# Performance work log

Hardware: AMD Instinct MI355X
Metric: run time of the kernel (lower is better)

## Reference

```python
import jax, jax.numpy as jnp
import numpy as np

N = 100000
F_IN = 128
HID = 128
NCLS = 40
NEG_SLOPE = 0.2
BN_EPS = 1e-5


def setup_inputs() -> dict:
    key = jax.random.key(0)
    ks = jax.random.split(key, 16)
    x = jax.random.normal(ks[0], (N, F_IN), dtype=jnp.float32)
    # self-loop-free random edges: dst = (src + 1 + r) % N
    E = 1600000
    src = jax.random.randint(ks[1], (E,), 0, N)
    off = jax.random.randint(ks[2], (E,), 1, N)
    dst = (src + off) % N
    edge_index = jnp.stack([src, dst]).astype(jnp.int64)

    def glorot(k, shape):
        fan = shape[0] + shape[-1]
        s = jnp.sqrt(6.0 / fan)
        return jax.random.uniform(k, shape, jnp.float32, -s, s)

    params = {
        'W1': glorot(ks[3], (F_IN, HID)),
        'as1': glorot(ks[4], (HID,)), 'ad1': glorot(ks[5], (HID,)),
        'b1': jnp.zeros((HID,), jnp.float32),
        'g1': jnp.ones((HID,), jnp.float32), 'beta1': jnp.zeros((HID,), jnp.float32),
        'W2': glorot(ks[6], (HID, HID)),
        'as2': glorot(ks[7], (HID,)), 'ad2': glorot(ks[8], (HID,)),
        'b2': jnp.zeros((HID,), jnp.float32),
        'g2': jnp.ones((HID,), jnp.float32), 'beta2': jnp.zeros((HID,), jnp.float32),
        'Wc': glorot(ks[9], (HID, NCLS)),
        'bc': jnp.zeros((NCLS,), jnp.float32),
    }
    return {'x': x, 'edge_index': edge_index, **params}


def _gat_conv(h_in, src, dst, W, a_src, a_dst, bias):
    # heads=1, concat=False -> single head, mean over heads is identity
    h = h_in @ W                               # [N, C]
    alpha_s = h @ a_src                        # [N]
    alpha_d = h @ a_dst                        # [N]
    alpha = alpha_s[src] + alpha_d[dst]        # [E] edge score
    alpha = jax.nn.leaky_relu(alpha, NEG_SLOPE)
    # segment softmax over destination node neighborhoods
    m = jax.ops.segment_max(alpha, dst, num_segments=N)
    e = jnp.exp(alpha - m[dst])
    s = jax.ops.segment_sum(e, dst, num_segments=N)
    alpha = e / s[dst]
    msg = h[src] * alpha[:, None]              # [E, C]
    out = jax.ops.segment_sum(msg, dst, num_segments=N)
    return out + bias


def _batchnorm(x, gamma, beta):
    mu = jnp.mean(x, axis=0)
    var = jnp.mean(jnp.square(x - mu), axis=0)  # biased, as torch BN training
    return (x - mu) * jax.lax.rsqrt(var + BN_EPS) * gamma + beta


def reference(x, edge_index, W1, as1, ad1, b1, g1, beta1,
              W2, as2, ad2, b2, g2, beta2, Wc, bc):
    src, dst = edge_index[0], edge_index[1]
    # add self loops (input edges are guaranteed self-loop-free)
    loop = jnp.arange(N, dtype=src.dtype)
    src = jnp.concatenate([src, loop])
    dst = jnp.concatenate([dst, loop])

    h = _gat_conv(x, src, dst, W1, as1, ad1, b1)
    h = jax.nn.relu(_batchnorm(h, g1, beta1))
    h = _gat_conv(h, src, dst, W2, as2, ad2, b2)
    h = jax.nn.relu(_batchnorm(h, g2, beta2))
    return h @ Wc + bc
```

## Files before the change

### kernel.cpp

```cpp
#include <hip/hip_runtime.h>
#include <hip/hip_fp16.h>
#include <math.h>


#define CDIM 128
#define NCLS_ 40
#define NEG_SLOPE_ 0.2f
#define BN_EPS_ 1e-5f
#define BRNG 256
#define BCAP 6144
#define EPB 16

using short8  = __attribute__((ext_vector_type(8))) short;
using short4v = __attribute__((ext_vector_type(4))) short;
using f32x4   = __attribute__((ext_vector_type(4))) float;

static __device__ __forceinline__ float lrelu(float a) {
    return a > 0.f ? a : NEG_SLOPE_ * a;
}
static __device__ __forceinline__ short f2bf(float f) {
    unsigned u = __float_as_uint(f);
    u += 0x7fffu + ((u >> 16) & 1u);
    return (short)(u >> 16);
}
static __device__ __forceinline__ float bf_lo(unsigned u) { return __uint_as_float(u << 16); }
static __device__ __forceinline__ float bf_hi(unsigned u) { return __uint_as_float(u & 0xffff0000u); }
static __device__ __forceinline__ __half2 u2h2(unsigned u) { return __builtin_bit_cast(__half2, u); }
static __device__ __forceinline__ unsigned h22u(__half2 h) { return __builtin_bit_cast(unsigned, h); }

__global__ void k_setup(int* bcur, float* bnsum, int NB, int n, int E, int* offs,
                        const float* __restrict__ W1, const float* __restrict__ W2,
                        const float* __restrict__ Wc,
                        short* __restrict__ Wt1, short* __restrict__ Wt2,
                        short* __restrict__ Wtc) {
    int i = blockIdx.x * blockDim.x + threadIdx.x;
    if (i < NB) bcur[i] = 0;
    if (i < 512) bnsum[i] = 0.f;
    if (i == 0) offs[n] = E + n;
    if (i < 128 * 128) {
        int k = i >> 7, nn = i & 127;
        Wt1[nn * 128 + k] = f2bf(W1[i]);
        Wt2[nn * 128 + k] = f2bf(W2[i]);
    }
    if (i < 48 * 128) {
        int nn = i >> 7, k = i & 127;
        Wtc[i] = (nn < NCLS_) ? f2bf(Wc[k * NCLS_ + nn]) : (short)0;
    }
}

__global__ __launch_bounds__(256) void k_binA(
    const int* __restrict__ src, const int* __restrict__ dst, int E,
    int* __restrict__ bcur, uint2* __restrict__ bucket, int NB)
{
    __shared__ int hist[400];
    __shared__ int base[400];
    int t = threadIdx.x;
    long e0 = (long)blockIdx.x * (256 * EPB) + t;

    for (int i = t; i < NB; i += 256) hist[i] = 0;
    __syncthreads();

    int sv[EPB], dv[EPB];
    #pragma unroll
    for (int i = 0; i < EPB; i++) {
        long e = e0 + (long)i * 256;
        if (e < E) {
            sv[i] = src[e]; dv[i] = dst[e];
            atomicAdd(&hist[dv[i] >> 8], 1);
        } else dv[i] = -1;
    }
    __syncthreads();

    for (int i = t; i < NB; i += 256) {
        int h = hist[i];
        base[i] = (h > 0) ? atomicAdd(&bcur[i], h) : 0;
    }
    __syncthreads();
    for (int i = t; i < NB; i += 256) hist[i] = 0;
    __syncthreads();

    #pragma unroll
    for (int i = 0; i < EPB; i++) {
        if (dv[i] >= 0) {
            int b = dv[i] >> 8;
            int pos = base[b] + atomicAdd(&hist[b], 1);
            if (pos < BCAP)
                bucket[(size_t)b * BCAP + pos] =
                    make_uint2((unsigned)sv[i], (unsigned)dv[i]);
        }
    }
}

__global__ __launch_bounds__(256) void k_fillB(
    const uint2* __restrict__ bucket, const int* __restrict__ bcur,
    int n, int NB, int* __restrict__ offs, int* __restrict__ csr)
{
    __shared__ int hist[256];
    __shared__ int scanb[256];
    __shared__ int cur[256];
    __shared__ int buf[BCAP + BRNG];
    int b = blockIdx.x, t = threadIdx.x;
    int node0 = b << 8;
    int nodesIn = min(BRNG, n - node0);
    int cnt = min(bcur[b], BCAP);
    const uint2* mybkt = bucket + (size_t)b * BCAP;

    int part = 0;
    for (int j = t; j < b; j += 256) part += min(bcur[j], BCAP);
    scanb[t] = part; __syncthreads();
    for (int s2 = 128; s2 > 0; s2 >>= 1) {
        if (t < s2) scanb[t] += scanb[t + s2];
        __syncthreads();
    }
    int base = scanb[0] + node0;
    __syncthreads();

    hist[t] = 0; __syncthreads();
    for (int e2 = t; e2 < cnt; e2 += 256)
        atomicAdd(&hist[mybkt[e2].y & 255], 1);
    __syncthreads();

    int v = hist[t] + ((t < nodesIn) ? 1 : 0);
    scanb[t] = v; __syncthreads();
    for (int d = 1; d < 256; d <<= 1) {
        int x2 = (t >= d) ? scanb[t - d] : 0;
        __syncthreads();
        scanb[t] += x2;
        __syncthreads();
    }
    int lo = scanb[t] - v;
    if (t < nodesIn) {
        offs[node0 + t] = base + lo;
        buf[lo] = node0 + t;
        cur[t] = lo + 1;
    }
    __syncthreads();

    for (int e2 = t; e2 < cnt; e2 += 256) {
        uint2 ed = mybkt[e2];
        int pos = atomicAdd(&cur[ed.y & 255], 1);
        buf[pos] = (int)ed.x;
    }
    __syncthreads();

    int tot = cnt + nodesIn;
    for (int j2 = t; j2 < tot; j2 += 256) csr[base + j2] = buf[j2];
}

__global__ __launch_bounds__(256) void k_gemm_mfma(
    const float* __restrict__ Xf, const unsigned* __restrict__ Xb,
    const short* __restrict__ Wt,
    const float* __restrict__ bnsum, const float* __restrict__ gamma,
    const float* __restrict__ beta, float invn,
    const float* __restrict__ av_s, const float* __restrict__ av_d,
    short* __restrict__ Hh, float* __restrict__ alpha_s, float* __restrict__ alpha_d,
    int n, int fuse)
{
    __shared__ short As[64 * 128];
    __shared__ short Bs[128 * 128];
    __shared__ float part_s[4][64];
    __shared__ float part_d[4][64];
    int t = threadIdx.x;
    int row0 = blockIdx.x * 64;

    for (int j = 0; j < 8; j++) {
        int idx = j * 256 + t;
        int nn = idx >> 4, cc = idx & 15;
        *(short8*)(Bs + nn * 128 + cc * 8) = *(const short8*)(Wt + nn * 128 + cc * 8);
    }
    float4 sc4 = make_float4(1.f, 1.f, 1.f, 1.f);
    float4 sh4 = make_float4(0.f, 0.f, 0.f, 0.f);
    if (fuse) {
        int cb = (t & 31) * 4;
        float4 s0 = *(const float4*)(bnsum + cb);
        float4 s1 = *(const float4*)(bnsum + 128 + cb);
        float4 gm = *(const float4*)(gamma + cb);
        float4 bt = *(const float4*)(beta + cb);
        float mean, var;
        mean = s0.x * invn; var = fmaxf(s1.x * invn - mean * mean, 0.f);
        sc4.x = gm.x * rsqrtf(var + BN_EPS_); sh4.x = bt.x - mean * sc4.x;
        mean = s0.y * invn; var = fmaxf(s1.y * invn - mean * mean, 0.f);
        sc4.y = gm.y * rsqrtf(var + BN_EPS_); sh4.y = bt.y - mean * sc4.y;
        mean = s0.z * invn; var = fmaxf(s1.z * invn - mean * mean, 0.f);
        sc4.z = gm.z * rsqrtf(var + BN_EPS_); sh4.z = bt.z - mean * sc4.z;
        mean = s0.w * invn; var = fmaxf(s1.w * invn - mean * mean, 0.f);
        sc4.w = gm.w * rsqrtf(var + BN_EPS_); sh4.w = bt.w - mean * sc4.w;
    }
    for (int j = 0; j < 8; j++) {
        int idx = j * 256 + t;
        int r = idx >> 5, k4 = idx & 31;
        int gr = row0 + r;
        float4 xv = make_float4(0.f, 0.f, 0.f, 0.f);
        if (fuse) {
            if (gr < n) {
                uint2 u = *(const uint2*)(Xb + (size_t)gr * 64 + k4 * 2);
                xv.x = bf_lo(u.x); xv.y = bf_hi(u.x);
                xv.z = bf_lo(u.y); xv.w = bf_hi(u.y);
            }
            xv.x = fmaxf(fmaf(xv.x, sc4.x, sh4.x), 0.f);
            xv.y = fmaxf(fmaf(xv.y, sc4.y, sh4.y), 0.f);
            xv.z = fmaxf(fmaf(xv.z, sc4.z, sh4.z), 0.f);
            xv.w = fmaxf(fmaf(xv.w, sc4.w, sh4.w), 0.f);
        } else {
            if (gr < n) xv = *(const float4*)(Xf + (size_t)gr * CDIM + k4 * 4);
        }
        short4v o;
        o.x = f2bf(xv.x); o.y = f2bf(xv.y); o.z = f2bf(xv.z); o.w = f2bf(xv.w);
        *(short4v*)(As + r * 128 + k4 * 4) = o;
    }
    __syncthreads();

    int w = t >> 6, lane = t & 63, q = lane >> 4, c = lane & 15;
    f32x4 zero = {0.f, 0.f, 0.f, 0.f};
    f32x4 acc[4][2];
    for (int i = 0; i < 4; i++) { acc[i][0] = zero; acc[i][1] = zero; }

    for (int ks = 0; ks < 4; ks++) {
        int k0 = ks * 32 + q * 8;
        short8 a0 = *(short8*)(As + (c) * 128 + k0);
        short8 a1 = *(short8*)(As + (16 + c) * 128 + k0);
        short8 a2 = *(short8*)(As + (32 + c) * 128 + k0);
        short8 a3 = *(short8*)(As + (48 + c) * 128 + k0);
        short8 b0 = *(short8*)(Bs + (w * 32 + c) * 128 + k0);
        short8 b1 = *(short8*)(Bs + (w * 32 + 16 + c) * 128 + k0);
        acc[0][0] = __builtin_amdgcn_mfma_f32_16x16x32_bf16(a0, b0, acc[0][0], 0, 0, 0);
        acc[1][0] = __builtin_amdgcn_mfma_f32_16x16x32_bf16(a1, b0, acc[1][0], 0, 0, 0);
        acc[2][0] = __builtin_amdgcn_mfma_f32_16x16x32_bf16(a2, b0, acc[2][0], 0, 0, 0);
        acc[3][0] = __builtin_amdgcn_mfma_f32_16x16x32_bf16(a3, b0, acc[3][0], 0, 0, 0);
        acc[0][1] = __builtin_amdgcn_mfma_f32_16x16x32_bf16(a0, b1, acc[0][1], 0, 0, 0);
        acc[1][1] = __builtin_amdgcn_mfma_f32_16x16x32_bf16(a1, b1, acc[1][1], 0, 0, 0);
        acc[2][1] = __builtin_amdgcn_mfma_f32_16x16x32_bf16(a2, b1, acc[2][1], 0, 0, 0);
        acc[3][1] = __builtin_amdgcn_mfma_f32_16x16x32_bf16(a3, b1, acc[3][1], 0, 0, 0);
    }

    float as0 = av_s[w * 32 + c],      as1 = av_s[w * 32 + 16 + c];
    float ad0 = av_d[w * 32 + c],      ad1 = av_d[w * 32 + 16 + c];
    #pragma unroll
    for (int mt = 0; mt < 4; mt++) {
        #pragma unroll
        for (int r = 0; r < 4; r++) {
            float v0 = acc[mt][0][r], v1 = acc[mt][1][r];
            float ps = v0 * as0 + v1 * as1;
            float pd = v0 * ad0 + v1 * ad1;
            #pragma unroll
            for (int off = 1; off < 16; off <<= 1) {
                ps += __shfl_xor(ps, off);
                pd += __shfl_xor(pd, off);
            }
            if (c == 0) {
                part_s[w][mt * 16 + q * 4 + r] = ps;
                part_d[w][mt * 16 + q * 4 + r] = pd;
            }
        }
    }
    __syncthreads();

    short* Hs = As;
    #pragma unroll
    for (int mt = 0; mt < 4; mt++)
        #pragma unroll
        for (int nt = 0; nt < 2; nt++)
            #pragma unroll
            for (int r = 0; r < 4; r++)
                Hs[(mt * 16 + q * 4 + r) * 128 + w * 32 + nt * 16 + c] =
                    (short)__half_as_ushort(__float2half_rn(acc[mt][nt][r]));

    if (t < 64) {
        int row = row0 + t;
        if (row < n) {
            alpha_s[row] = part_s[0][t] + part_s[1][t] + part_s[2][t] + part_s[3][t];
            alpha_d[row] = part_d[0][t] + part_d[1][t] + part_d[2][t] + part_d[3][t];
        }
    }
    __syncthreads();

    for (int j = 0; j < 4; j++) {
        int idx = j * 256 + t;
        int r = idx >> 4, cc = idx & 15;
        int gr = row0 + r;
        if (gr < n)
            *(short8*)(Hh + (size_t)gr * 128 + cc * 8) = *(short8*)(Hs + r * 128 + cc * 8);
    }
}

__global__ __launch_bounds__(256) void k_agg(
    const unsigned* __restrict__ Hh, const int* __restrict__ offs,
    const int* __restrict__ csr, const float* __restrict__ alpha_s,
    const float* __restrict__ alpha_d, const float* __restrict__ bias,
    unsigned* __restrict__ Ob, int n)
{
    int i = blockIdx.x * 4 + (threadIdx.x >> 6);
    int lane = threadIdx.x & 63;
    if (i >= n) return;
    int o0 = offs[i], o1 = offs[i + 1];
    float adi = alpha_d[i];

    float m = -1e30f;
    float se = 0.f;
    __half2 acc2 = __floats2half2_rn(0.f, 0.f);

    for (int c0 = o0; c0 < o1; c0 += 64) {
        int j = c0 + lane;
        int cnt = min(64, o1 - c0);
        int sj = (j < o1) ? csr[j] : 0;
        float a = (j < o1) ? lrelu(alpha_s[sj] + adi) : -1e30f;

        float cm = a;
        #pragma unroll
        for (int o = 32; o > 0; o >>= 1) cm = fmaxf(cm, __shfl_xor(cm, o));
        if (cm > m) {
            float r = __expf(m - cm);
            se *= r;
            acc2 = __hmul2(acc2, __float2half2_rn(r));
            m = cm;
        }
        float wl = (j < o1) ? __expf(a - m) : 0.f;
        se += wl;
        int wli = (int)h22u(__float2half2_rn(wl));

        for (int b = 0; b < cnt; b += 8) {
            unsigned u[8]; int wb[8];
            #pragma unroll
            for (int q2 = 0; q2 < 8; q2++) {
                int el = min(b + q2, 63);
                int s = __builtin_amdgcn_readlane(sj, el);
                wb[q2] = __builtin_amdgcn_readlane(wli, el);
                u[q2] = Hh[(size_t)(unsigned)s * 64 + lane];
            }
            #pragma unroll
            for (int q2 = 0; q2 < 8; q2++) {
                acc2 = __hfma2(u2h2(u[q2]), u2h2((unsigned)wb[q2]), acc2);
            }
        }
    }

    #pragma unroll
    for (int o = 32; o > 0; o >>= 1) se += __shfl_xor(se, o);
    float inv = 1.f / se;
    float2 af = __half22float2(acc2);
    float2 b2 = *(const float2*)(bias + lane * 2);
    float rx = fmaf(af.x, inv, b2.x);
    float ry = fmaf(af.y, inv, b2.y);
    unsigned pack = ((unsigned)(unsigned short)f2bf(ry) << 16) |
                    (unsigned)(unsigned short)f2bf(rx);
    Ob[(size_t)i * 64 + lane] = pack;
}

__global__ void k_bnstats(const unsigned* __restrict__ Hb, int n, float* __restrict__ sums) {
    __shared__ float red[4][64][4];
    int w = threadIdx.x & 63;
    int g = threadIdx.x >> 6;
    float slo = 0.f, shi = 0.f, qlo = 0.f, qhi = 0.f;
    for (int r = blockIdx.x * 4 + g; r < n; r += gridDim.x * 4) {
        unsigned u = Hb[(size_t)r * 64 + w];
        float lo = bf_lo(u), hi = bf_hi(u);
        slo += lo; shi += hi; qlo += lo * lo; qhi += hi * hi;
    }
    red[g][w][0] = slo; red[g][w][1] = shi; red[g][w][2] = qlo; red[g][w][3] = qhi;
    __syncthreads();
    if (threadIdx.x < 64) {
        int w2 = threadIdx.x;
        float s0 = 0.f, s1 = 0.f, s2 = 0.f, s3 = 0.f;
        for (int gg = 0; gg < 4; gg++) {
            s0 += red[gg][w2][0]; s1 += red[gg][w2][1];
            s2 += red[gg][w2][2]; s3 += red[gg][w2][3];
        }
        atomicAdd(&sums[2 * w2], s0);
        atomicAdd(&sums[2 * w2 + 1], s1);
        atomicAdd(&sums[128 + 2 * w2], s2);
        atomicAdd(&sums[128 + 2 * w2 + 1], s3);
    }
}

__global__ __launch_bounds__(256) void k_cls(
    const unsigned* __restrict__ G, const short* __restrict__ Wtc,
    const float* __restrict__ bc, const float* __restrict__ bnsum,
    const float* __restrict__ gamma, const float* __restrict__ beta, float invn,
    float* __restrict__ out, int n)
{
    __shared__ short As[64 * 128];
    __shared__ short Bs[48 * 128];
    int t = threadIdx.x;
    int row0 = blockIdx.x * 64;

    for (int j = 0; j < 3; j++) {
        int idx = j * 256 + t;
        *(short8*)(Bs + idx * 8) = *(const short8*)(Wtc + idx * 8);
    }
    float4 sc4, sh4;
    {
        int cb = (t & 31) * 4;
        float4 s0 = *(const float4*)(bnsum + cb);
        float4 s1 = *(const float4*)(bnsum + 128 + cb);
        float4 gm = *(const float4*)(gamma + cb);
        float4 bt = *(const float4*)(beta + cb);
        float mean, var;
        mean = s0.x * invn; var = fmaxf(s1.x * invn - mean * mean, 0.f);
        sc4.x = gm.x * rsqrtf(var + BN_EPS_); sh4.x = bt.x - mean * sc4.x;
        mean = s0.y * invn; var = fmaxf(s1.y * invn - mean * mean, 0.f);
        sc4.y = gm.y * rsqrtf(var + BN_EPS_); sh4.y = bt.y - mean * sc4.y;
        mean = s0.z * invn; var = fmaxf(s1.z * invn - mean * mean, 0.f);
        sc4.z = gm.z * rsqrtf(var + BN_EPS_); sh4.z = bt.z - mean * sc4.z;
        mean = s0.w * invn; var = fmaxf(s1.w * invn - mean * mean, 0.f);
        sc4.w = gm.w * rsqrtf(var + BN_EPS_); sh4.w = bt.w - mean * sc4.w;
    }
    for (int j = 0; j < 8; j++) {
        int idx = j * 256 + t;
        int r = idx >> 5, k4 = idx & 31;
        int gr = row0 + r;
        float4 xv = make_float4(0.f, 0.f, 0.f, 0.f);
        if (gr < n) {
            uint2 u = *(const uint2*)(G + (size_t)gr * 64 + k4 * 2);
            xv.x = bf_lo(u.x); xv.y = bf_hi(u.x);
            xv.z = bf_lo(u.y); xv.w = bf_hi(u.y);
        }
        xv.x = fmaxf(fmaf(xv.x, sc4.x, sh4.x), 0.f);
        xv.y = fmaxf(fmaf(xv.y, sc4.y, sh4.y), 0.f);
        xv.z = fmaxf(fmaf(xv.z, sc4.z, sh4.z), 0.f);
        xv.w = fmaxf(fmaf(xv.w, sc4.w, sh4.w), 0.f);
        short4v o;
        o.x = f2bf(xv.x); o.y = f2bf(xv.y); o.z = f2bf(xv.z); o.w = f2bf(xv.w);
        *(short4v*)(As + r * 128 + k4 * 4) = o;
    }
    __syncthreads();

    int w = t >> 6, lane = t & 63, q = lane >> 4, c = lane & 15;
    f32x4 zero = {0.f, 0.f, 0.f, 0.f};
    f32x4 acc[3] = {zero, zero, zero};
    for (int ks = 0; ks < 4; ks++) {
        int k0 = ks * 32 + q * 8;
        short8 a  = *(short8*)(As + (w * 16 + c) * 128 + k0);
        short8 b0 = *(short8*)(Bs + (c) * 128 + k0);
        short8 b1 = *(short8*)(Bs + (16 + c) * 128 + k0);
        short8 b2 = *(short8*)(Bs + (32 + c) * 128 + k0);
        acc[0] = __builtin_amdgcn_mfma_f32_16x16x32_bf16(a, b0, acc[0], 0, 0, 0);
        acc[1] = __builtin_amdgcn_mfma_f32_16x16x32_bf16(a, b1, acc[1], 0, 0, 0);
        acc[2] = __builtin_amdgcn_mfma_f32_16x16x32_bf16(a, b2, acc[2], 0, 0, 0);
    }
    float bc0 = bc[c], bc1 = bc[16 + c], bc2 = (c < 8) ? bc[32 + c] : 0.f;
    #pragma unroll
    for (int r = 0; r < 4; r++) {
        int row = row0 + w * 16 + q * 4 + r;
        if (row < n) {
            out[(size_t)row * NCLS_ + c]      = acc[0][r] + bc0;
            out[(size_t)row * NCLS_ + 16 + c] = acc[1][r] + bc1;
            if (c < 8) out[(size_t)row * NCLS_ + 32 + c] = acc[2][r] + bc2;
        }
    }
}

extern "C" void kernel_launch(void* const* d_in, const int* in_sizes, int n_in,
                              void* d_out, int out_size, void* d_ws, size_t ws_size,
                              hipStream_t stream)
{
    const float* x   = (const float*)d_in[0];
    const int*   ei  = (const int*)d_in[1];
    const float* W1  = (const float*)d_in[2];
    const float* as1 = (const float*)d_in[3];
    const float* ad1 = (const float*)d_in[4];
    const float* b1  = (const float*)d_in[5];
    const float* g1  = (const float*)d_in[6];
    const float* be1 = (const float*)d_in[7];
    const float* W2  = (const float*)d_in[8];
    const float* as2 = (const float*)d_in[9];
    const float* ad2 = (const float*)d_in[10];
    const float* b2  = (const float*)d_in[11];
    const float* g2  = (const float*)d_in[12];
    const float* be2 = (const float*)d_in[13];
    const float* Wc  = (const float*)d_in[14];
    const float* bc  = (const float*)d_in[15];
    float* out = (float*)d_out;

    int n = in_sizes[0] / CDIM;
    int E = in_sizes[1] / 2;
    const int* src = ei;
    const int* dst = ei + E;
    float invn = 1.f / (float)n;
    int NB = (n + BRNG - 1) / BRNG;

    char* p = (char*)d_ws;
    auto alloc = [&p](size_t bytes) { char* q = p; p += (bytes + 63) & ~(size_t)63; return q; };
    short*    Hh      = (short*)alloc((size_t)n * CDIM * sizeof(short));
    unsigned* bufB    = (unsigned*)alloc((size_t)n * 64 * sizeof(unsigned));
    float*    alpha_s = (float*)alloc((size_t)n * sizeof(float));
    float*    alpha_d = (float*)alloc((size_t)n * sizeof(float));
    float*    bnsum   = (float*)alloc(512 * sizeof(float));
    short*    Wt1     = (short*)alloc(128 * 128 * sizeof(short));
    short*    Wt2     = (short*)alloc(128 * 128 * sizeof(short));
    short*    Wtc     = (short*)alloc(48 * 128 * sizeof(short));
    int*      bcurs   = (int*)alloc((size_t)NB * sizeof(int));
    int*      offs    = (int*)alloc((size_t)(n + 1) * sizeof(int));
    uint2*    bucket  = (uint2*)alloc((size_t)NB * BCAP * sizeof(uint2));
    int*      csr     = (int*)alloc((size_t)(E + n) * sizeof(int));

    k_setup<<<dim3(64), dim3(256), 0, stream>>>(bcurs, bnsum, NB, n, E, offs,
                                                W1, W2, Wc, Wt1, Wt2, Wtc);
    k_binA<<<dim3((E + 4095) / 4096), dim3(256), 0, stream>>>(src, dst, E, bcurs, bucket, NB);
    k_fillB<<<dim3(NB), dim3(256), 0, stream>>>(bucket, bcurs, n, NB, offs, csr);

    dim3 ggrid((n + 63) / 64);
    dim3 wgrid((n + 3) / 4);

    k_gemm_mfma<<<ggrid, 256, 0, stream>>>(x, nullptr, Wt1, nullptr, nullptr, nullptr,
                                           invn, as1, ad1, Hh, alpha_s, alpha_d, n, 0);
    k_agg<<<wgrid, 256, 0, stream>>>((const unsigned*)Hh, offs, csr, alpha_s, alpha_d,
                                     b1, bufB, n);
    k_bnstats<<<dim3(256), dim3(256), 0, stream>>>(bufB, n, bnsum);

    k_gemm_mfma<<<ggrid, 256, 0, stream>>>(nullptr, bufB, Wt2, bnsum, g1, be1,
                                           invn, as2, ad2, Hh, alpha_s, alpha_d, n, 1);
    k_agg<<<wgrid, 256, 0, stream>>>((const unsigned*)Hh, offs, csr, alpha_s, alpha_d,
                                     b2, bufB, n);
    k_bnstats<<<dim3(256), dim3(256), 0, stream>>>(bufB, n, bnsum + 256);

    k_cls<<<ggrid, 256, 0, stream>>>(bufB, Wtc, bc, bnsum + 256, g2, be2, invn, out, n);
}
```

Before: 443.1 us.

## Vectorize GAT aggregation gathers and pack bucket edges into one word

The aggregation kernel now splits each wavefront into four 16-lane groups. Each group gathers a full 256-byte neighbor row with 16-byte loads and processes four edges per round, with the (src, weight) pairs staged in shared memory instead of passed via readlane. Partial half2 sums are then combined across the groups with shuffles. Separately, the edge bucket stores src<<8 | local dst in one 32-bit word instead of a uint2, halving the bucket traffic, though this assumes src fits in 24 bits.

```diff
diff --git a/kernel.cpp b/kernel.cpp
--- a/kernel.cpp
+++ b/kernel.cpp
@@ -50,7 +50,7 @@
 
 __global__ __launch_bounds__(256) void k_binA(
     const int* __restrict__ src, const int* __restrict__ dst, int E,
-    int* __restrict__ bcur, uint2* __restrict__ bucket, int NB)
+    int* __restrict__ bcur, unsigned* __restrict__ bucket, int NB)
 {
     __shared__ int hist[400];
     __shared__ int base[400];
@@ -86,13 +86,13 @@
             int pos = base[b] + atomicAdd(&hist[b], 1);
             if (pos < BCAP)
                 bucket[(size_t)b * BCAP + pos] =
-                    make_uint2((unsigned)sv[i], (unsigned)dv[i]);
+                    ((unsigned)sv[i] << 8) | ((unsigned)dv[i] & 255u);
         }
     }
 }
 
 __global__ __launch_bounds__(256) void k_fillB(
-    const uint2* __restrict__ bucket, const int* __restrict__ bcur,
+    const unsigned* __restrict__ bucket, const int* __restrict__ bcur,
     int n, int NB, int* __restrict__ offs, int* __restrict__ csr)
 {
     __shared__ int hist[256];
@@ -103,7 +103,7 @@
     int node0 = b << 8;
     int nodesIn = min(BRNG, n - node0);
     int cnt = min(bcur[b], BCAP);
-    const uint2* mybkt = bucket + (size_t)b * BCAP;
+    const unsigned* mybkt = bucket + (size_t)b * BCAP;
 
     int part = 0;
     for (int j = t; j < b; j += 256) part += min(bcur[j], BCAP);
@@ -117,7 +117,7 @@
 
     hist[t] = 0; __syncthreads();
     for (int e2 = t; e2 < cnt; e2 += 256)
-        atomicAdd(&hist[mybkt[e2].y & 255], 1);
+        atomicAdd(&hist[mybkt[e2] & 255u], 1);
     __syncthreads();
 
     int v = hist[t] + ((t < nodesIn) ? 1 : 0);
@@ -137,9 +137,9 @@
     __syncthreads();
 
     for (int e2 = t; e2 < cnt; e2 += 256) {
-        uint2 ed = mybkt[e2];
-        int pos = atomicAdd(&cur[ed.y & 255], 1);
-        buf[pos] = (int)ed.x;
+        unsigned ed = mybkt[e2];
+        int pos = atomicAdd(&cur[ed & 255u], 1);
+        buf[pos] = (int)(ed >> 8);
     }
     __syncthreads();
 
@@ -284,20 +284,22 @@
 }
 
 __global__ __launch_bounds__(256) void k_agg(
-    const unsigned* __restrict__ Hh, const int* __restrict__ offs,
+    const uint4* __restrict__ Hh4, const int* __restrict__ offs,
     const int* __restrict__ csr, const float* __restrict__ alpha_s,
     const float* __restrict__ alpha_d, const float* __restrict__ bias,
-    unsigned* __restrict__ Ob, int n)
+    uint4* __restrict__ Ob4, int n)
 {
-    int i = blockIdx.x * 4 + (threadIdx.x >> 6);
+    __shared__ uint2 pairs[4][64];
+    int wid = threadIdx.x >> 6;
     int lane = threadIdx.x & 63;
+    int i = blockIdx.x * 4 + wid;
     if (i >= n) return;
     int o0 = offs[i], o1 = offs[i + 1];
     float adi = alpha_d[i];
-
-    float m = -1e30f;
-    float se = 0.f;
-    __half2 acc2 = __floats2half2_rn(0.f, 0.f);
+    int q = lane >> 4, sl = lane & 15;
+
+    float m = -1e30f, se = 0.f;
+    __half2 ac0 = __float2half2_rn(0.f), ac1 = ac0, ac2 = ac0, ac3 = ac0;
 
     for (int c0 = o0; c0 < o1; c0 += 64) {
         int j = c0 + lane;
@@ -311,39 +313,69 @@
         if (cm > m) {
             float r = __expf(m - cm);
             se *= r;
-            acc2 = __hmul2(acc2, __float2half2_rn(r));
+            __half2 r2 = __float2half2_rn(r);
+            ac0 = __hmul2(ac0, r2); ac1 = __hmul2(ac1, r2);
+            ac2 = __hmul2(ac2, r2); ac3 = __hmul2(ac3, r2);
             m = cm;
         }
         float wl = (j < o1) ? __expf(a - m) : 0.f;
         se += wl;
-        int wli = (int)h22u(__float2half2_rn(wl));
-
-        for (int b = 0; b < cnt; b += 8) {
-            unsigned u[8]; int wb[8];
-            #pragma unroll
-            for (int q2 = 0; q2 < 8; q2++) {
-                int el = min(b + q2, 63);
-                int s = __builtin_amdgcn_readlane(sj, el);
-                wb[q2] = __builtin_amdgcn_readlane(wli, el);
-                u[q2] = Hh[(size_t)(unsigned)s * 64 + lane];
-            }
-            #pragma unroll
-            for (int q2 = 0; q2 < 8; q2++) {
-                acc2 = __hfma2(u2h2(u[q2]), u2h2((unsigned)wb[q2]), acc2);
-            }
+        pairs[wid][lane] = make_uint2((unsigned)sj, h22u(__float2half2_rn(wl)));
+
+        int rounds = (cnt + 3) >> 2;
+        int r = 0;
+        for (; r + 2 <= rounds; r += 2) {
+            uint2 pA = pairs[wid][r * 4 + q];
+            uint2 pB = pairs[wid][r * 4 + 4 + q];
+            uint4 uA = Hh4[(size_t)pA.x * 16 + sl];
+            uint4 uB = Hh4[(size_t)pB.x * 16 + sl];
+            __half2 wA = u2h2(pA.y), wB = u2h2(pB.y);
+            ac0 = __hfma2(u2h2(uA.x), wA, ac0);
+            ac1 = __hfma2(u2h2(uA.y), wA, ac1);
+            ac2 = __hfma2(u2h2(uA.z), wA, ac2);
+            ac3 = __hfma2(u2h2(uA.w), wA, ac3);
+            ac0 = __hfma2(u2h2(uB.x), wB, ac0);
+            ac1 = __hfma2(u2h2(uB.y), wB, ac1);
+            ac2 = __hfma2(u2h2(uB.z), wB, ac2);
+            ac3 = __hfma2(u2h2(uB.w), wB, ac3);
+        }
+        if (r < rounds) {
+            uint2 p = pairs[wid][r * 4 + q];
+            uint4 u = Hh4[(size_t)p.x * 16 + sl];
+            __half2 w2 = u2h2(p.y);
+            ac0 = __hfma2(u2h2(u.x), w2, ac0);
+            ac1 = __hfma2(u2h2(u.y), w2, ac1);
+            ac2 = __hfma2(u2h2(u.z), w2, ac2);
+            ac3 = __hfma2(u2h2(u.w), w2, ac3);
         }
     }
 
     #pragma unroll
     for (int o = 32; o > 0; o >>= 1) se += __shfl_xor(se, o);
     float inv = 1.f / se;
-    float2 af = __half22float2(acc2);
-    float2 b2 = *(const float2*)(bias + lane * 2);
-    float rx = fmaf(af.x, inv, b2.x);
-    float ry = fmaf(af.y, inv, b2.y);
-    unsigned pack = ((unsigned)(unsigned short)f2bf(ry) << 16) |
-                    (unsigned)(unsigned short)f2bf(rx);
-    Ob[(size_t)i * 64 + lane] = pack;
+
+    #define COMB(h) \
+        h = __hadd2(h, u2h2((unsigned)__shfl_xor((int)h22u(h), 16))); \
+        h = __hadd2(h, u2h2((unsigned)__shfl_xor((int)h22u(h), 32)));
+    COMB(ac0) COMB(ac1) COMB(ac2) COMB(ac3)
+    #undef COMB
+
+    if (q == 0) {
+        float4 b0 = *(const float4*)(bias + sl * 8);
+        float4 b1 = *(const float4*)(bias + sl * 8 + 4);
+        float2 f0 = __half22float2(ac0), f1 = __half22float2(ac1);
+        float2 f2 = __half22float2(ac2), f3 = __half22float2(ac3);
+        uint4 pk;
+        pk.x = ((unsigned)(unsigned short)f2bf(fmaf(f0.y, inv, b0.y)) << 16) |
+               (unsigned)(unsigned short)f2bf(fmaf(f0.x, inv, b0.x));
+        pk.y = ((unsigned)(unsigned short)f2bf(fmaf(f1.y, inv, b0.w)) << 16) |
+               (unsigned)(unsigned short)f2bf(fmaf(f1.x, inv, b0.z));
+        pk.z = ((unsigned)(unsigned short)f2bf(fmaf(f2.y, inv, b1.y)) << 16) |
+               (unsigned)(unsigned short)f2bf(fmaf(f2.x, inv, b1.x));
+        pk.w = ((unsigned)(unsigned short)f2bf(fmaf(f3.y, inv, b1.w)) << 16) |
+               (unsigned)(unsigned short)f2bf(fmaf(f3.x, inv, b1.z));
+        Ob4[(size_t)i * 16 + sl] = pk;
+    }
 }
 
 __global__ void k_bnstats(const unsigned* __restrict__ Hb, int n, float* __restrict__ sums) {
@@ -490,7 +522,7 @@
     short*    Wtc     = (short*)alloc(48 * 128 * sizeof(short));
     int*      bcurs   = (int*)alloc((size_t)NB * sizeof(int));
     int*      offs    = (int*)alloc((size_t)(n + 1) * sizeof(int));
-    uint2*    bucket  = (uint2*)alloc((size_t)NB * BCAP * sizeof(uint2));
+    unsigned* bucket  = (unsigned*)alloc((size_t)NB * BCAP * sizeof(unsigned));
     int*      csr     = (int*)alloc((size_t)(E + n) * sizeof(int));
 
     k_setup<<<dim3(64), dim3(256), 0, stream>>>(bcurs, bnsum, NB, n, E, offs,
@@ -503,14 +535,14 @@
 
     k_gemm_mfma<<<ggrid, 256, 0, stream>>>(x, nullptr, Wt1, nullptr, nullptr, nullptr,
                                            invn, as1, ad1, Hh, alpha_s, alpha_d, n, 0);
-    k_agg<<<wgrid, 256, 0, stream>>>((const unsigned*)Hh, offs, csr, alpha_s, alpha_d,
-                                     b1, bufB, n);
+    k_agg<<<wgrid, 256, 0, stream>>>((const uint4*)Hh, offs, csr, alpha_s, alpha_d,
+                                     b1, (uint4*)bufB, n);
     k_bnstats<<<dim3(256), dim3(256), 0, stream>>>(bufB, n, bnsum);
 
     k_gemm_mfma<<<ggrid, 256, 0, stream>>>(nullptr, bufB, Wt2, bnsum, g1, be1,
                                            invn, as2, ad2, Hh, alpha_s, alpha_d, n, 1);
-    k_agg<<<wgrid, 256, 0, stream>>>((const unsigned*)Hh, offs, csr, alpha_s, alpha_d,
-                                     b2, bufB, n);
+    k_agg<<<wgrid, 256, 0, stream>>>((const uint4*)Hh, offs, csr, alpha_s, alpha_d,
+                                     b2, (uint4*)bufB, n);
     k_bnstats<<<dim3(256), dim3(256), 0, stream>>>(bufB, n, bnsum + 256);
 
     k_cls<<<ggrid, 256, 0, stream>>>(bufB, Wtc, bc, bnsum + 256, g2, be2, invn, out, n);
```

After: 444.4 us. No clear change (+0.3%).
